# Optimization experiments

Measured on AMD Instinct MI355X. Metric: run time of the kernel, lower is better.

Reference implementation:

```python
import jax, jax.numpy as jnp
import numpy as np

N, S, Z, H, K, DEG = 8192, 4, 64, 128, 4, 16
E = N * DEG


def setup_inputs() -> dict:
    key = jax.random.key(0)
    ks = jax.random.split(key, 9)
    g = lambda k, shape, scale=1.0: jax.random.normal(k, shape, dtype=jnp.float32) * scale
    return dict(
        zIG=g(ks[0], (N, S, Z)),                         # node intention features
        xt_enc=g(ks[1], (N, S, H)),                      # encoded actions per node
        Ws=g(ks[2], (K, H, Z), 1.0 / np.sqrt(Z)),        # attn_s[k] weights (no bias)
        Wd=g(ks[3], (K, H, Z), 1.0 / np.sqrt(Z)),        # attn_d[k] weights
        F2_w1=g(ks[4], (H, 2 * H), 1.0 / np.sqrt(2 * H)),
        F2_w2=g(ks[5], (H, H), 1.0 / np.sqrt(H)),
        F1_w1=g(ks[6], (H, K * H), 1.0 / np.sqrt(K * H)),
        F1_w2=g(ks[7], (H, H), 1.0 / np.sqrt(H)),
        src=jax.random.randint(ks[8], (E,), 0, N),       # random source per edge
        dst=jnp.repeat(jnp.arange(N), DEG),              # regular graph: DEG in-edges per node, grouped
    )


def reference(zIG, xt_enc, Ws, Wd, F2_w1, F2_w2, F1_w1, F1_w2, src, dst):
    n, s, h = xt_enc.shape
    k = Ws.shape[0]
    deg = src.shape[0] // n

    # ---- edge_attention: eIG[e,s,k] = leaky_relu(sum_h (Ws_k z_src)*(Wd_k z_dst)) ----
    zs, zd = zIG[src], zIG[dst]                          # [E,S,Z] irregular gathers
    scores = []
    for kk in range(k):                                  # k is small & structural
        a_s = zs @ Ws[kk].T                              # [E,S,H]
        a_d = zd @ Wd[kk].T                              # [E,S,H]
        scores.append(jax.nn.leaky_relu((a_s * a_d).sum(-1)))  # [E,S]
    eIG = jnp.stack(scores, axis=-1)                     # [E,S,K]

    # ---- message_func: dA = F2(cat(xt_src, xt_dst)) ----
    msg_in = jnp.concatenate([xt_enc[src], xt_enc[dst]], axis=-1)   # [E,S,2H]
    dA = jax.nn.relu(msg_in @ F2_w1.T) @ F2_w2.T                    # [E,S,H]

    # ---- reduce_func: softmax over neighbor mailbox (dim=1), weighted mean ----
    # dst is grouped with constant degree, so the DGL mailbox is a reshape.
    alpha = jax.nn.softmax(eIG.reshape(n, deg, s, k), axis=1)       # [N,D,S,K]
    mail = dA.reshape(n, deg, s, h)                                 # [N,D,S,H]
    res = jnp.einsum('ndsk,ndsh->nskh', alpha, mail) / deg          # mean over D
    res = res.reshape(n, s, k * h)                                  # cat over k (k-major)
    deltax = jax.nn.relu(res @ F1_w1.T) @ F1_w2.T                   # [N,S,H]
    return deltax, alpha
```

## Files before the change

kernel.cpp:

```cpp
#include <hip/hip_runtime.h>
#include <hip/hip_bf16.h>

typedef unsigned short u16;
typedef unsigned int u32;
typedef unsigned long long u64;
using ushort8 = __attribute__((ext_vector_type(8))) unsigned short;
using short8  = __attribute__((ext_vector_type(8))) short;
using f32x4   = __attribute__((ext_vector_type(4))) float;

__device__ __forceinline__ float bf2f(u16 v) {
  union { u32 u; float f; } x; x.u = ((u32)v) << 16; return x.f;
}
__device__ __forceinline__ float u2f(u32 u) {
  union { u32 u; float f; } x; x.u = u; return x.f;
}
__device__ __forceinline__ u16 f2bf(float f) {
  union { u32 u; float f; } x; x.f = f;
  u32 r = x.u + 0x7FFFu + ((x.u >> 16) & 1u);
  return (u16)(r >> 16);
}
__device__ __forceinline__ u32 pack2bf(float lo, float hi) {
  return (u32)f2bf(lo) | ((u32)f2bf(hi) << 16);
}
__device__ __forceinline__ void split8(const float* ap, short8& hi, short8& lo) {
  float4 a0 = *(const float4*)ap, a1 = *(const float4*)(ap + 4);
  float e[8] = {a0.x, a0.y, a0.z, a0.w, a1.x, a1.y, a1.z, a1.w};
  u16 h[8], l[8];
  #pragma unroll
  for (int j = 0; j < 8; ++j) {
    u32 b = __float_as_uint(e[j]);
    h[j] = (u16)(b >> 16);
    l[j] = f2bf(e[j] - u2f(b & 0xffff0000u));
  }
  hi = *(short8*)h; lo = *(short8*)l;
}
__device__ __forceinline__ void stage_w(const float* g, int stride, int c, u16* Wl, int t) {
  int row = t >> 1, half = t & 1;
  const float4* gp = (const float4*)(g + (size_t)row * stride + c * 64 + half * 32);
  ushort8* d = (ushort8*)(Wl + row * 72 + half * 32);
  #pragma unroll
  for (int i = 0; i < 4; ++i) {
    float4 a = gp[2 * i], b = gp[2 * i + 1];
    ushort8 o;
    o[0] = f2bf(a.x); o[1] = f2bf(a.y); o[2] = f2bf(a.z); o[3] = f2bf(a.w);
    o[4] = f2bf(b.x); o[5] = f2bf(b.y); o[6] = f2bf(b.z); o[7] = f2bf(b.w);
    d[i] = o;
  }
}
__device__ __forceinline__ void stage_w512(const float* g, int stride, int c, u16* Wl, int t) {
  int row = t >> 2, q = t & 3;
  const float4* gp = (const float4*)(g + (size_t)row * stride + c * 64 + q * 16);
  ushort8* d = (ushort8*)(Wl + row * 72 + q * 16);
  #pragma unroll
  for (int i = 0; i < 2; ++i) {
    float4 a = gp[2 * i], b = gp[2 * i + 1];
    ushort8 o;
    o[0] = f2bf(a.x); o[1] = f2bf(a.y); o[2] = f2bf(a.z); o[3] = f2bf(a.w);
    o[4] = f2bf(b.x); o[5] = f2bf(b.y); o[6] = f2bf(b.z); o[7] = f2bf(b.w);
    d[i] = o;
  }
}

__global__ __launch_bounds__(256) void k_prep(const float* __restrict__ Ws,
                                              const float* __restrict__ Wd,
                                              const float* __restrict__ F1w1,
                                              const float* __restrict__ F2w2,
                                              const float* __restrict__ zIG,
                                              u16* __restrict__ Bh, u16* __restrict__ Bl,
                                              float* __restrict__ WW2,
                                              u16* __restrict__ zh, u16* __restrict__ zl) {
  if (blockIdx.x < 64) {
    int t = blockIdx.x * 256 + threadIdx.x;
    int k = t >> 12, z1 = (t >> 6) & 63, z2 = t & 63;
    const float* wsp = Ws + k * 8192 + z1;
    const float* wdp = Wd + k * 8192 + z2;
    float acc = 0.f;
    #pragma unroll 8
    for (int h = 0; h < 128; ++h) acc += wsp[h * 64] * wdp[h * 64];
    u32 b = __float_as_uint(acc);
    Bh[(k * 64 + z1) * 64 + z2] = (u16)(b >> 16);
    Bl[(k * 64 + z1) * 64 + z2] = f2bf(acc - u2f(b & 0xffff0000u));
  } else if (blockIdx.x < 320) {
    int id = (blockIdx.x - 64) * 256 + threadIdx.x;
    int ho = id >> 9, kk = (id >> 7) & 3, hi = id & 127;
    const float* wa = F1w1 + ho * 512 + kk * 128;
    const float* wb = F2w2 + hi;
    float acc = 0.f;
    #pragma unroll 8
    for (int j = 0; j < 128; ++j) acc += wa[j] * wb[j * 128];
    WW2[ho * 512 + kk * 128 + hi] = acc * 0.0625f;
  } else {
    int base = (blockIdx.x - 320) * 256 + threadIdx.x;
    #pragma unroll
    for (int i = 0; i < 16; ++i) {
      int idx = base + i * 32768;
      float4 zv = ((const float4*)zIG)[idx];
      float e[4] = {zv.x, zv.y, zv.z, zv.w};
      u16 h[4], l[4];
      #pragma unroll
      for (int j = 0; j < 4; ++j) {
        u32 b = __float_as_uint(e[j]);
        h[j] = (u16)(b >> 16);
        l[j] = f2bf(e[j] - u2f(b & 0xffff0000u));
      }
      *(u64*)&zh[idx * 4] = *(u64*)h;
      *(u64*)&zl[idx * 4] = *(u64*)l;
    }
  }
}

__global__ __launch_bounds__(256) void k_tduv(const float* __restrict__ zIG,
                                              const u16* __restrict__ Bh_g,
                                              const u16* __restrict__ Bl_g,
                                              const float* __restrict__ xt,
                                              const float* __restrict__ W1,
                                              u16* __restrict__ tdh, u16* __restrict__ tdl,
                                              u16* __restrict__ u, u16* __restrict__ v) {
  __shared__ __align__(16) u16 SM[128 * 72];
  int t = threadIdx.x, lane = t & 63, w = t >> 6;
  int l15 = lane & 15, kc = lane >> 4;
  if (blockIdx.x < 1024) {
    u16* Bh = SM;
    u16* Bl = SM + 64 * 72;
    int cq = blockIdx.x & 3;
    size_t rowbase = (size_t)(blockIdx.x >> 2) * 128 + w * 32;
    {
      int row = t >> 2, q = t & 3;
      const ushort8* gh = (const ushort8*)(Bh_g + (cq * 64 + row) * 64 + q * 16);
      const ushort8* gl = (const ushort8*)(Bl_g + (cq * 64 + row) * 64 + q * 16);
      ushort8* dh = (ushort8*)(Bh + row * 72 + q * 16);
      ushort8* dl = (ushort8*)(Bl + row * 72 + q * 16);
      dh[0] = gh[0]; dh[1] = gh[1];
      dl[0] = gl[0]; dl[1] = gl[1];
    }
    __syncthreads();
    f32x4 acc[2][4];
    #pragma unroll
    for (int mt = 0; mt < 2; ++mt)
      #pragma unroll
      for (int nt = 0; nt < 4; ++nt) acc[mt][nt] = (f32x4){0.f, 0.f, 0.f, 0.f};
    #pragma unroll
    for (int ks = 0; ks < 2; ++ks) {
      short8 ah[2], al[2];
      #pragma unroll
      for (int mt = 0; mt < 2; ++mt)
        split8(zIG + (rowbase + mt * 16 + l15) * 64 + ks * 32 + kc * 8, ah[mt], al[mt]);
      #pragma unroll
      for (int nt = 0; nt < 4; ++nt) {
        int bo = (nt * 16 + l15) * 72 + ks * 32 + kc * 8;
        short8 bh = *(const short8*)&Bh[bo];
        short8 bl = *(const short8*)&Bl[bo];
        #pragma unroll
        for (int mt = 0; mt < 2; ++mt) {
          acc[mt][nt] = __builtin_amdgcn_mfma_f32_16x16x32_bf16(ah[mt], bh, acc[mt][nt], 0, 0, 0);
          acc[mt][nt] = __builtin_amdgcn_mfma_f32_16x16x32_bf16(al[mt], bh, acc[mt][nt], 0, 0, 0);
          acc[mt][nt] = __builtin_amdgcn_mfma_f32_16x16x32_bf16(ah[mt], bl, acc[mt][nt], 0, 0, 0);
        }
      }
    }
    #pragma unroll
    for (int mt = 0; mt < 2; ++mt)
      #pragma unroll
      for (int nt = 0; nt < 4; ++nt)
        #pragma unroll
        for (int j = 0; j < 4; ++j) {
          float val = acc[mt][nt][j];
          size_t idx = (rowbase + mt * 16 + kc * 4 + j) * 256 + cq * 64 + nt * 16 + l15;
          u32 b = __float_as_uint(val);
          tdh[idx] = (u16)(b >> 16);
          tdl[idx] = f2bf(val - u2f(b & 0xffff0000u));
        }
  } else {
    u16* Wl = SM;
    int bid2 = blockIdx.x - 1024;
    int sel = bid2 >> 8;
    size_t rowbase = (size_t)(bid2 & 255) * 128 + w * 32;
    const float* Wbase = W1 + sel * 128;
    f32x4 acc[2][8];
    #pragma unroll
    for (int mt = 0; mt < 2; ++mt)
      #pragma unroll
      for (int nt = 0; nt < 8; ++nt) acc[mt][nt] = (f32x4){0.f, 0.f, 0.f, 0.f};
    for (int c = 0; c < 2; ++c) {
      __syncthreads();
      stage_w(Wbase, 256, c, Wl, t);
      __syncthreads();
      #pragma unroll
      for (int ks = 0; ks < 2; ++ks) {
        short8 af[2];
        #pragma unroll
        for (int mt = 0; mt < 2; ++mt) {
          const float* ap = xt + (rowbase + mt * 16 + l15) * 128 + c * 64 + ks * 32 + kc * 8;
          float4 a0 = *(const float4*)ap, a1 = *(const float4*)(ap + 4);
          u16 tmp[8] = {f2bf(a0.x), f2bf(a0.y), f2bf(a0.z), f2bf(a0.w),
                        f2bf(a1.x), f2bf(a1.y), f2bf(a1.z), f2bf(a1.w)};
          af[mt] = *(short8*)tmp;
        }
        #pragma unroll
        for (int nt = 0; nt < 8; ++nt) {
          short8 bw = *(const short8*)&Wl[(nt * 16 + l15) * 72 + ks * 32 + kc * 8];
          #pragma unroll
          for (int mt = 0; mt < 2; ++mt)
            acc[mt][nt] = __builtin_amdgcn_mfma_f32_16x16x32_bf16(af[mt], bw, acc[mt][nt], 0, 0, 0);
        }
      }
    }
    u16* dstp = sel ? v : u;
    #pragma unroll
    for (int mt = 0; mt < 2; ++mt)
      #pragma unroll
      for (int nt = 0; nt < 8; ++nt)
        #pragma unroll
        for (int j = 0; j < 4; ++j)
          dstp[(rowbase + mt * 16 + kc * 4 + j) * 128 + nt * 16 + l15] =
              f2bf(acc[mt][nt][j]);
  }
}

__global__ __launch_bounds__(256) void k_score(
    const u16* __restrict__ zh, const u16* __restrict__ zl,
    const u16* __restrict__ tdh, const u16* __restrict__ tdl,
    const int* __restrict__ src, const u16* __restrict__ uW, const u16* __restrict__ vW,
    float* __restrict__ out, u16* __restrict__ m_ws) {
  __shared__ float a20[4][320];

  int t = threadIdx.x, lane = t & 63, w = t >> 6;
  int n = blockIdx.x * 4 + w;
  int l15 = lane & 15, lq = lane >> 4;

  const u16* tdh_n = tdh + (size_t)n * 1024;
  const u16* tdl_n = tdl + (size_t)n * 1024;
  short8 bh0 = *(const short8*)(tdh_n + l15 * 64 + lq * 8);
  short8 bh1 = *(const short8*)(tdh_n + l15 * 64 + 32 + lq * 8);
  short8 bl0 = *(const short8*)(tdl_n + l15 * 64 + lq * 8);
  short8 bl1 = *(const short8*)(tdl_n + l15 * 64 + 32 + lq * 8);
  size_t zrow = (size_t)src[n * 16 + l15] * 256;
  f32x4 acc[4];
  #pragma unroll
  for (int s = 0; s < 4; ++s) {
    short8 ah0 = *(const short8*)(zh + zrow + s * 64 + lq * 8);
    short8 ah1 = *(const short8*)(zh + zrow + s * 64 + 32 + lq * 8);
    short8 al0 = *(const short8*)(zl + zrow + s * 64 + lq * 8);
    short8 al1 = *(const short8*)(zl + zrow + s * 64 + 32 + lq * 8);
    f32x4 a = (f32x4){0.f, 0.f, 0.f, 0.f};
    a = __builtin_amdgcn_mfma_f32_16x16x32_bf16(ah0, bh0, a, 0, 0, 0);
    a = __builtin_amdgcn_mfma_f32_16x16x32_bf16(ah1, bh1, a, 0, 0, 0);
    a = __builtin_amdgcn_mfma_f32_16x16x32_bf16(al0, bh0, a, 0, 0, 0);
    a = __builtin_amdgcn_mfma_f32_16x16x32_bf16(al1, bh1, a, 0, 0, 0);
    a = __builtin_amdgcn_mfma_f32_16x16x32_bf16(ah0, bl0, a, 0, 0, 0);
    a = __builtin_amdgcn_mfma_f32_16x16x32_bf16(ah1, bl1, a, 0, 0, 0);
    acc[s] = a;
  }
  int qsel = l15 >> 2;
  float sc[4];
  #pragma unroll
  for (int j = 0; j < 4; ++j) {
    float a01 = (qsel == 0) ? acc[0][j] : acc[1][j];
    float a23 = (qsel == 2) ? acc[2][j] : acc[3][j];
    float vsc = (qsel < 2) ? a01 : a23;
    sc[j] = vsc > 0.f ? vsc : 0.01f * vsc;
  }
  float mx = fmaxf(fmaxf(sc[0], sc[1]), fmaxf(sc[2], sc[3]));
  mx = fmaxf(mx, __shfl_xor(mx, 16));
  mx = fmaxf(mx, __shfl_xor(mx, 32));
  float e0 = __expf(sc[0] - mx), e1 = __expf(sc[1] - mx);
  float e2 = __expf(sc[2] - mx), e3 = __expf(sc[3] - mx);
  float esum = (e0 + e1) + (e2 + e3);
  esum += __shfl_xor(esum, 16);
  esum += __shfl_xor(esum, 32);
  float inv = 1.0f / esum;
  float al[4] = {e0 * inv, e1 * inv, e2 * inv, e3 * inv};
  {
    float* ob = out + 4194304u + (unsigned)n * 256;
    #pragma unroll
    for (int j = 0; j < 4; ++j) {
      int d = lq * 4 + j;
      ob[d * 16 + l15] = al[j];
      a20[w][d * 20 + l15] = al[j];
    }
  }
  __syncthreads();
  int sidx[16];
  #pragma unroll
  for (int dd = 0; dd < 16; ++dd) sidx[dd] = src[n * 16 + dd];
  const u32* up = (const u32*)uW;
  u32* mp = (u32*)(m_ws + (size_t)n * 2048);
  #pragma unroll
  for (int s = 0; s < 4; ++s) {
    u32 vb = *(const u32*)(vW + (size_t)n * 512 + s * 128 + lane * 2);
    float v_lo = u2f(vb << 16), v_hi = u2f(vb & 0xffff0000u);
    u32 ub[16];
    #pragma unroll
    for (int dd = 0; dd < 16; ++dd)
      ub[dd] = up[(size_t)sidx[dd] * 256 + s * 64 + lane];
    float m0l = 0.f, m0h = 0.f, m1l = 0.f, m1h = 0.f;
    float m2l = 0.f, m2h = 0.f, m3l = 0.f, m3h = 0.f;
    #pragma unroll
    for (int dd = 0; dd < 16; ++dd) {
      float r_lo = fmaxf(u2f(ub[dd] << 16) + v_lo, 0.f);
      float r_hi = fmaxf(u2f(ub[dd] & 0xffff0000u) + v_hi, 0.f);
      float4 a = *(const float4*)&a20[w][dd * 20 + s * 4];
      m0l += a.x * r_lo; m0h += a.x * r_hi;
      m1l += a.y * r_lo; m1h += a.y * r_hi;
      m2l += a.z * r_lo; m2h += a.z * r_hi;
      m3l += a.w * r_lo; m3h += a.w * r_hi;
    }
    mp[(s * 4 + 0) * 64 + lane] = pack2bf(m0l, m0h);
    mp[(s * 4 + 1) * 64 + lane] = pack2bf(m1l, m1h);
    mp[(s * 4 + 2) * 64 + lane] = pack2bf(m2l, m2h);
    mp[(s * 4 + 3) * 64 + lane] = pack2bf(m3l, m3h);
  }
}

__global__ __launch_bounds__(512) void k_fg(const u16* __restrict__ A,
                                            const float* __restrict__ WF,
                                            const float* __restrict__ WG,
                                            float* __restrict__ out) {
  __shared__ u16 Wl[128 * 72];
  __shared__ u16 hidl[128 * 136];
  int t = threadIdx.x, lane = t & 63, w = t >> 6;
  size_t rowbase = (size_t)blockIdx.x * 128 + w * 16;
  int l15 = lane & 15, kc = lane >> 4;
  f32x4 acc[8];
  #pragma unroll
  for (int nt = 0; nt < 8; ++nt) acc[nt] = (f32x4){0.f, 0.f, 0.f, 0.f};
  for (int c = 0; c < 8; ++c) {
    __syncthreads();
    stage_w512(WF, 512, c, Wl, t);
    __syncthreads();
    #pragma unroll
    for (int ks = 0; ks < 2; ++ks) {
      short8 af = *(const short8*)(A + (rowbase + l15) * 512 + c * 64 + ks * 32 + kc * 8);
      #pragma unroll
      for (int nt = 0; nt < 8; ++nt) {
        short8 bf = *(const short8*)&Wl[(nt * 16 + l15) * 72 + ks * 32 + kc * 8];
        acc[nt] = __builtin_amdgcn_mfma_f32_16x16x32_bf16(af, bf, acc[nt], 0, 0, 0);
      }
    }
  }
  #pragma unroll
  for (int nt = 0; nt < 8; ++nt)
    #pragma unroll
    for (int j = 0; j < 4; ++j)
      hidl[(w * 16 + kc * 4 + j) * 136 + nt * 16 + l15] = f2bf(fmaxf(acc[nt][j], 0.f));
  f32x4 acc2[8];
  #pragma unroll
  for (int nt = 0; nt < 8; ++nt) acc2[nt] = (f32x4){0.f, 0.f, 0.f, 0.f};
  for (int c = 0; c < 2; ++c) {
    __syncthreads();
    stage_w512(WG, 128, c, Wl, t);
    __syncthreads();
    #pragma unroll
    for (int ks = 0; ks < 2; ++ks) {
      short8 af = *(const short8*)&hidl[(w * 16 + l15) * 136 + c * 64 + ks * 32 + kc * 8];
      #pragma unroll
      for (int nt = 0; nt < 8; ++nt) {
        short8 bf = *(const short8*)&Wl[(nt * 16 + l15) * 72 + ks * 32 + kc * 8];
        acc2[nt] = __builtin_amdgcn_mfma_f32_16x16x32_bf16(af, bf, acc2[nt], 0, 0, 0);
      }
    }
  }
  #pragma unroll
  for (int nt = 0; nt < 8; ++nt)
    #pragma unroll
    for (int j = 0; j < 4; ++j)
      out[(rowbase + kc * 4 + j) * 128 + nt * 16 + l15] = acc2[nt][j];
}

extern "C" void kernel_launch(void* const* d_in, const int* in_sizes, int n_in,
                              void* d_out, int out_size, void* d_ws, size_t ws_size,
                              hipStream_t stream) {
  const float* zIG  = (const float*)d_in[0];
  const float* xt   = (const float*)d_in[1];
  const float* Ws   = (const float*)d_in[2];
  const float* Wd   = (const float*)d_in[3];
  const float* F2w1 = (const float*)d_in[4];
  const float* F2w2 = (const float*)d_in[5];
  const float* F1w1 = (const float*)d_in[6];
  const float* F1w2 = (const float*)d_in[7];
  const int* src    = (const int*)d_in[8];
  float* out = (float*)d_out;

  char* ws = (char*)d_ws;
  u16* Bh    = (u16*)ws;
  u16* Bl    = (u16*)(ws + 32768);
  u16* tdh   = (u16*)(ws + 65536);
  u16* tdl   = (u16*)(ws + 16842752);
  u16* u     = (u16*)(ws + 33619968);
  u16* v     = (u16*)(ws + 42008576);
  u16* zh    = (u16*)(ws + 50397184);
  u16* zl    = (u16*)(ws + 54591488);
  float* WW2 = (float*)(ws + 58785792);
  u16* m     = (u16*)(ws + 59047936);

  k_prep <<<448,  256, 0, stream>>>(Ws, Wd, F1w1, F2w2, zIG, Bh, Bl, WW2, zh, zl);
  k_tduv <<<1536, 256, 0, stream>>>(zIG, Bh, Bl, xt, F2w1, tdh, tdl, u, v);
  k_score<<<2048, 256, 0, stream>>>(zh, zl, tdh, tdl, src, u, v, out, m);
  k_fg   <<<256,  512, 0, stream>>>(m, WW2, F1w2, out);
}
```

Baseline: 100.9 us.

## Fuse destination-side bilinear transform into score kernel, dropping td workspace

The per-node zIG·B product (td) is now computed on the fly inside the score kernel with MFMA and kept in shared memory, instead of being written to global memory by a separate kernel as hi/lo bf16 pairs and read back. The src indices for the block are also staged once in shared memory. This removes a large global write and read of the td tensor in exchange for more MFMA work and shared-memory traffic per score block. The prep kernel gains an unused dead-code branch with a stray extern declaration, which looks like leftover scaffolding.

Measured after the change: 101.8 us. Within noise of the previous version (+0.9%).

```diff
diff --git a/kernel.cpp b/kernel.cpp
--- a/kernel.cpp
+++ b/kernel.cpp
@@ -61,17 +61,18 @@
   }
 }
 
-__global__ __launch_bounds__(256) void k_prep(const float* __restrict__ Ws,
-                                              const float* __restrict__ Wd,
-                                              const float* __restrict__ F1w1,
-                                              const float* __restrict__ F2w2,
-                                              const float* __restrict__ zIG,
-                                              u16* __restrict__ Bh, u16* __restrict__ Bl,
-                                              float* __restrict__ WW2,
-                                              u16* __restrict__ zh, u16* __restrict__ zl) {
+__global__ __launch_bounds__(256) void k_prepuv(
+    const float* __restrict__ Ws, const float* __restrict__ Wd,
+    const float* __restrict__ F1w1, const float* __restrict__ F2w2,
+    const float* __restrict__ zIG, const float* __restrict__ xt,
+    u16* __restrict__ Bh, u16* __restrict__ Bl, float* __restrict__ WW2,
+    u16* __restrict__ zh, u16* __restrict__ zl,
+    u16* __restrict__ u, u16* __restrict__ v) {
+  __shared__ __align__(16) u16 SM[128 * 72];
+  int t = threadIdx.x;
   if (blockIdx.x < 64) {
-    int t = blockIdx.x * 256 + threadIdx.x;
-    int k = t >> 12, z1 = (t >> 6) & 63, z2 = t & 63;
+    int id = blockIdx.x * 256 + t;
+    int k = id >> 12, z1 = (id >> 6) & 63, z2 = id & 63;
     const float* wsp = Ws + k * 8192 + z1;
     const float* wdp = Wd + k * 8192 + z2;
     float acc = 0.f;
@@ -81,7 +82,7 @@
     Bh[(k * 64 + z1) * 64 + z2] = (u16)(b >> 16);
     Bl[(k * 64 + z1) * 64 + z2] = f2bf(acc - u2f(b & 0xffff0000u));
   } else if (blockIdx.x < 320) {
-    int id = (blockIdx.x - 64) * 256 + threadIdx.x;
+    int id = (blockIdx.x - 64) * 256 + t;
     int ho = id >> 9, kk = (id >> 7) & 3, hi = id & 127;
     const float* wa = F1w1 + ho * 512 + kk * 128;
     const float* wb = F2w2 + hi;
@@ -89,8 +90,8 @@
     #pragma unroll 8
     for (int j = 0; j < 128; ++j) acc += wa[j] * wb[j * 128];
     WW2[ho * 512 + kk * 128 + hi] = acc * 0.0625f;
-  } else {
-    int base = (blockIdx.x - 320) * 256 + threadIdx.x;
+  } else if (blockIdx.x < 448) {
+    int base = (blockIdx.x - 320) * 256 + t;
     #pragma unroll
     for (int i = 0; i < 16; ++i) {
       int idx = base + i * 32768;
@@ -106,135 +107,119 @@
       *(u64*)&zh[idx * 4] = *(u64*)h;
       *(u64*)&zl[idx * 4] = *(u64*)l;
     }
-  }
-}
-
-__global__ __launch_bounds__(256) void k_tduv(const float* __restrict__ zIG,
-                                              const u16* __restrict__ Bh_g,
-                                              const u16* __restrict__ Bl_g,
-                                              const float* __restrict__ xt,
-                                              const float* __restrict__ W1,
-                                              u16* __restrict__ tdh, u16* __restrict__ tdl,
-                                              u16* __restrict__ u, u16* __restrict__ v) {
-  __shared__ __align__(16) u16 SM[128 * 72];
+  } else {
+    int lane = t & 63, w = t >> 6;
+    int l15 = lane & 15, kc = lane >> 4;
+    int bid2 = blockIdx.x - 448;
+    int sel = bid2 >> 8;
+    size_t rowbase = (size_t)(bid2 & 255) * 128 + w * 32;
+    const float* Wbase = F1w1;
+    (void)Wbase;
+    const float* W1p = xt;
+    (void)W1p;
+    const float* F2w1 = (const float*)__builtin_assume_aligned((const void*)Ws, 16);
+    (void)F2w1;
+    extern __device__ void __chipstub();
+    (void)sel; (void)rowbase; (void)l15; (void)kc; (void)SM;
+  }
+}
+
+__global__ __launch_bounds__(256) void k_uv(const float* __restrict__ xt,
+                                            const float* __restrict__ W1,
+                                            u16* __restrict__ u, u16* __restrict__ v) {
+  __shared__ __align__(16) u16 Wl[128 * 72];
   int t = threadIdx.x, lane = t & 63, w = t >> 6;
   int l15 = lane & 15, kc = lane >> 4;
-  if (blockIdx.x < 1024) {
-    u16* Bh = SM;
-    u16* Bl = SM + 64 * 72;
-    int cq = blockIdx.x & 3;
-    size_t rowbase = (size_t)(blockIdx.x >> 2) * 128 + w * 32;
-    {
-      int row = t >> 2, q = t & 3;
-      const ushort8* gh = (const ushort8*)(Bh_g + (cq * 64 + row) * 64 + q * 16);
-      const ushort8* gl = (const ushort8*)(Bl_g + (cq * 64 + row) * 64 + q * 16);
-      ushort8* dh = (ushort8*)(Bh + row * 72 + q * 16);
-      ushort8* dl = (ushort8*)(Bl + row * 72 + q * 16);
-      dh[0] = gh[0]; dh[1] = gh[1];
-      dl[0] = gl[0]; dl[1] = gl[1];
-    }
-    __syncthreads();
-    f32x4 acc[2][4];
-    #pragma unroll
-    for (int mt = 0; mt < 2; ++mt)
-      #pragma unroll
-      for (int nt = 0; nt < 4; ++nt) acc[mt][nt] = (f32x4){0.f, 0.f, 0.f, 0.f};
+  int sel = blockIdx.x >> 8;
+  size_t rowbase = (size_t)(blockIdx.x & 255) * 128 + w * 32;
+  const float* Wbase = W1 + sel * 128;
+  f32x4 acc[2][8];
+  #pragma unroll
+  for (int mt = 0; mt < 2; ++mt)
+    #pragma unroll
+    for (int nt = 0; nt < 8; ++nt) acc[mt][nt] = (f32x4){0.f, 0.f, 0.f, 0.f};
+  for (int c = 0; c < 2; ++c) {
+    __syncthreads();
+    stage_w(Wbase, 256, c, Wl, t);
+    __syncthreads();
     #pragma unroll
     for (int ks = 0; ks < 2; ++ks) {
-      short8 ah[2], al[2];
-      #pragma unroll
-      for (int mt = 0; mt < 2; ++mt)
-        split8(zIG + (rowbase + mt * 16 + l15) * 64 + ks * 32 + kc * 8, ah[mt], al[mt]);
-      #pragma unroll
-      for (int nt = 0; nt < 4; ++nt) {
-        int bo = (nt * 16 + l15) * 72 + ks * 32 + kc * 8;
-        short8 bh = *(const short8*)&Bh[bo];
-        short8 bl = *(const short8*)&Bl[bo];
+      short8 af[2];
+      #pragma unroll
+      for (int mt = 0; mt < 2; ++mt) {
+        const float* ap = xt + (rowbase + mt * 16 + l15) * 128 + c * 64 + ks * 32 + kc * 8;
+        float4 a0 = *(const float4*)ap, a1 = *(const float4*)(ap + 4);
+        u16 tmp[8] = {f2bf(a0.x), f2bf(a0.y), f2bf(a0.z), f2bf(a0.w),
+                      f2bf(a1.x), f2bf(a1.y), f2bf(a1.z), f2bf(a1.w)};
+        af[mt] = *(short8*)tmp;
+      }
+      #pragma unroll
+      for (int nt = 0; nt < 8; ++nt) {
+        short8 bw = *(const short8*)&Wl[(nt * 16 + l15) * 72 + ks * 32 + kc * 8];
         #pragma unroll
-        for (int mt = 0; mt < 2; ++mt) {
-          acc[mt][nt] = __builtin_amdgcn_mfma_f32_16x16x32_bf16(ah[mt], bh, acc[mt][nt], 0, 0, 0);
-          acc[mt][nt] = __builtin_amdgcn_mfma_f32_16x16x32_bf16(al[mt], bh, acc[mt][nt], 0, 0, 0);
-          acc[mt][nt] = __builtin_amdgcn_mfma_f32_16x16x32_bf16(ah[mt], bl, acc[mt][nt], 0, 0, 0);
-        }
-      }
-    }
-    #pragma unroll
-    for (int mt = 0; mt < 2; ++mt)
-      #pragma unroll
-      for (int nt = 0; nt < 4; ++nt)
-        #pragma unroll
-        for (int j = 0; j < 4; ++j) {
-          float val = acc[mt][nt][j];
-          size_t idx = (rowbase + mt * 16 + kc * 4 + j) * 256 + cq * 64 + nt * 16 + l15;
-          u32 b = __float_as_uint(val);
-          tdh[idx] = (u16)(b >> 16);
-          tdl[idx] = f2bf(val - u2f(b & 0xffff0000u));
-        }
-  } else {
-    u16* Wl = SM;
-    int bid2 = blockIdx.x - 1024;
-    int sel = bid2 >> 8;
-    size_t rowbase = (size_t)(bid2 & 255) * 128 + w * 32;
-    const float* Wbase = W1 + sel * 128;
-    f32x4 acc[2][8];
-    #pragma unroll
-    for (int mt = 0; mt < 2; ++mt)
-      #pragma unroll
-      for (int nt = 0; nt < 8; ++nt) acc[mt][nt] = (f32x4){0.f, 0.f, 0.f, 0.f};
-    for (int c = 0; c < 2; ++c) {
-      __syncthreads();
-      stage_w(Wbase, 256, c, Wl, t);
-      __syncthreads();
-      #pragma unroll
-      for (int ks = 0; ks < 2; ++ks) {
-        short8 af[2];
-        #pragma unroll
-        for (int mt = 0; mt < 2; ++mt) {
-          const float* ap = xt + (rowbase + mt * 16 + l15) * 128 + c * 64 + ks * 32 + kc * 8;
-          float4 a0 = *(const float4*)ap, a1 = *(const float4*)(ap + 4);
-          u16 tmp[8] = {f2bf(a0.x), f2bf(a0.y), f2bf(a0.z), f2bf(a0.w),
-                        f2bf(a1.x), f2bf(a1.y), f2bf(a1.z), f2bf(a1.w)};
-          af[mt] = *(short8*)tmp;
-        }
-        #pragma unroll
-        for (int nt = 0; nt < 8; ++nt) {
-          short8 bw = *(const short8*)&Wl[(nt * 16 + l15) * 72 + ks * 32 + kc * 8];
-          #pragma unroll
-          for (int mt = 0; mt < 2; ++mt)
-            acc[mt][nt] = __builtin_amdgcn_mfma_f32_16x16x32_bf16(af[mt], bw, acc[mt][nt], 0, 0, 0);
-        }
-      }
-    }
-    u16* dstp = sel ? v : u;
-    #pragma unroll
-    for (int mt = 0; mt < 2; ++mt)
-      #pragma unroll
-      for (int nt = 0; nt < 8; ++nt)
-        #pragma unroll
-        for (int j = 0; j < 4; ++j)
-          dstp[(rowbase + mt * 16 + kc * 4 + j) * 128 + nt * 16 + l15] =
-              f2bf(acc[mt][nt][j]);
-  }
+        for (int mt = 0; mt < 2; ++mt)
+          acc[mt][nt] = __builtin_amdgcn_mfma_f32_16x16x32_bf16(af[mt], bw, acc[mt][nt], 0, 0, 0);
+      }
+    }
+  }
+  u16* dstp = sel ? v : u;
+  #pragma unroll
+  for (int mt = 0; mt < 2; ++mt)
+    #pragma unroll
+    for (int nt = 0; nt < 8; ++nt)
+      #pragma unroll
+      for (int j = 0; j < 4; ++j)
+        dstp[(rowbase + mt * 16 + kc * 4 + j) * 128 + nt * 16 + l15] =
+            f2bf(acc[mt][nt][j]);
 }
 
 __global__ __launch_bounds__(256) void k_score(
+    const float* __restrict__ zIG,
     const u16* __restrict__ zh, const u16* __restrict__ zl,
-    const u16* __restrict__ tdh, const u16* __restrict__ tdl,
+    const u16* __restrict__ Bh_g, const u16* __restrict__ Bl_g,
     const int* __restrict__ src, const u16* __restrict__ uW, const u16* __restrict__ vW,
     float* __restrict__ out, u16* __restrict__ m_ws) {
+  __shared__ float tdL[4][16 * 68];
   __shared__ float a20[4][320];
+  __shared__ int srcIdx[64];
 
   int t = threadIdx.x, lane = t & 63, w = t >> 6;
-  int n = blockIdx.x * 4 + w;
+  int n0 = blockIdx.x * 4;
+  int n = n0 + w;
   int l15 = lane & 15, lq = lane >> 4;
 
-  const u16* tdh_n = tdh + (size_t)n * 1024;
-  const u16* tdl_n = tdl + (size_t)n * 1024;
-  short8 bh0 = *(const short8*)(tdh_n + l15 * 64 + lq * 8);
-  short8 bh1 = *(const short8*)(tdh_n + l15 * 64 + 32 + lq * 8);
-  short8 bl0 = *(const short8*)(tdl_n + l15 * 64 + lq * 8);
-  short8 bl1 = *(const short8*)(tdl_n + l15 * 64 + 32 + lq * 8);
-  size_t zrow = (size_t)src[n * 16 + l15] * 256;
+  if (t < 64) srcIdx[t] = src[n0 * 16 + t];
+
+  {
+    f32x4 acc[4];
+    #pragma unroll
+    for (int nt = 0; nt < 4; ++nt) acc[nt] = (f32x4){0.f, 0.f, 0.f, 0.f};
+    #pragma unroll
+    for (int ch = 0; ch < 2; ++ch) {
+      short8 ah, al;
+      split8(zIG + (size_t)(n0 + (l15 >> 2)) * 256 + (l15 & 3) * 64 + ch * 32 + lq * 8,
+             ah, al);
+      #pragma unroll
+      for (int nt = 0; nt < 4; ++nt) {
+        const short8 bh = *(const short8*)(Bh_g + (w * 64 + nt * 16 + l15) * 64 + ch * 32 + lq * 8);
+        const short8 bl = *(const short8*)(Bl_g + (w * 64 + nt * 16 + l15) * 64 + ch * 32 + lq * 8);
+        acc[nt] = __builtin_amdgcn_mfma_f32_16x16x32_bf16(ah, bh, acc[nt], 0, 0, 0);
+        acc[nt] = __builtin_amdgcn_mfma_f32_16x16x32_bf16(al, bh, acc[nt], 0, 0, 0);
+        acc[nt] = __builtin_amdgcn_mfma_f32_16x16x32_bf16(ah, bl, acc[nt], 0, 0, 0);
+      }
+    }
+    #pragma unroll
+    for (int nt = 0; nt < 4; ++nt)
+      #pragma unroll
+      for (int j = 0; j < 4; ++j)
+        tdL[lq][(j * 4 + w) * 68 + nt * 16 + l15] = acc[nt][j];
+  }
+  __syncthreads();
+
+  short8 bh0, bl0, bh1, bl1;
+  split8(&tdL[w][l15 * 68 + lq * 8], bh0, bl0);
+  split8(&tdL[w][l15 * 68 + 32 + lq * 8], bh1, bl1);
+  size_t zrow = (size_t)srcIdx[w * 16 + l15] * 256;
   f32x4 acc[4];
   #pragma unroll
   for (int s = 0; s < 4; ++s) {
@@ -269,20 +254,17 @@
   esum += __shfl_xor(esum, 16);
   esum += __shfl_xor(esum, 32);
   float inv = 1.0f / esum;
-  float al[4] = {e0 * inv, e1 * inv, e2 * inv, e3 * inv};
+  float al_[4] = {e0 * inv, e1 * inv, e2 * inv, e3 * inv};
   {
     float* ob = out + 4194304u + (unsigned)n * 256;
     #pragma unroll
     for (int j = 0; j < 4; ++j) {
       int d = lq * 4 + j;
-      ob[d * 16 + l15] = al[j];
-      a20[w][d * 20 + l15] = al[j];
+      ob[d * 16 + l15] = al_[j];
+      a20[w][d * 20 + l15] = al_[j];
     }
   }
   __syncthreads();
-  int sidx[16];
-  #pragma unroll
-  for (int dd = 0; dd < 16; ++dd) sidx[dd] = src[n * 16 + dd];
   const u32* up = (const u32*)uW;
   u32* mp = (u32*)(m_ws + (size_t)n * 2048);
   #pragma unroll
@@ -292,7 +274,7 @@
     u32 ub[16];
     #pragma unroll
     for (int dd = 0; dd < 16; ++dd)
-      ub[dd] = up[(size_t)sidx[dd] * 256 + s * 64 + lane];
+      ub[dd] = up[(size_t)srcIdx[w * 16 + dd] * 256 + s * 64 + lane];
     float m0l = 0.f, m0h = 0.f, m1l = 0.f, m1h = 0.f;
     float m2l = 0.f, m2h = 0.f, m3l = 0.f, m3h = 0.f;
     #pragma unroll
@@ -384,17 +366,16 @@
   char* ws = (char*)d_ws;
   u16* Bh    = (u16*)ws;
   u16* Bl    = (u16*)(ws + 32768);
-  u16* tdh   = (u16*)(ws + 65536);
-  u16* tdl   = (u16*)(ws + 16842752);
-  u16* u     = (u16*)(ws + 33619968);
-  u16* v     = (u16*)(ws + 42008576);
-  u16* zh    = (u16*)(ws + 50397184);
-  u16* zl    = (u16*)(ws + 54591488);
-  float* WW2 = (float*)(ws + 58785792);
-  u16* m     = (u16*)(ws + 59047936);
-
-  k_prep <<<448,  256, 0, stream>>>(Ws, Wd, F1w1, F2w2, zIG, Bh, Bl, WW2, zh, zl);
-  k_tduv <<<1536, 256, 0, stream>>>(zIG, Bh, Bl, xt, F2w1, tdh, tdl, u, v);
-  k_score<<<2048, 256, 0, stream>>>(zh, zl, tdh, tdl, src, u, v, out, m);
-  k_fg   <<<256,  512, 0, stream>>>(m, WW2, F1w2, out);
-}
+  u16* u     = (u16*)(ws + 65536);
+  u16* v     = (u16*)(ws + 8454144);
+  u16* zh    = (u16*)(ws + 16842752);
+  u16* zl    = (u16*)(ws + 21037056);
+  float* WW2 = (float*)(ws + 25231360);
+  u16* m     = (u16*)(ws + 25493504);
+
+  k_prepuv<<<448,  256, 0, stream>>>(Ws, Wd, F1w1, F2w2, zIG, xt,
+                                     Bh, Bl, WW2, zh, zl, u, v);
+  k_uv    <<<512,  256, 0, stream>>>(xt, F2w1, u, v);
+  k_score <<<2048, 256, 0, stream>>>(zIG, zh, zl, Bh, Bl, src, u, v, out, m);
+  k_fg    <<<256,  512, 0, stream>>>(m, WW2, F1w2, out);
+}
```
